# Optimization experiments

Hardware: AMD Instinct MI355X
Metric: run time of the kernel (lower is better)

The kernel has to match this reference:

```python
import jax, jax.numpy as jnp
import numpy as np
from jax import lax

B, S, T = 128, 512, 256


def setup_inputs() -> dict:
    key = jax.random.key(0)
    k1, k2, k3, k4, k5, k6 = jax.random.split(key, 6)
    logits = jax.random.normal(k1, (B, S, T), dtype=jnp.float32)
    lengths = jax.random.randint(k2, (B,), S // 2, S + 1)
    mask = jnp.arange(S)[None, :] < lengths[:, None]  # [B,S] bool, mask[:,0] always True
    labels = jax.random.randint(k3, (B, S), 0, T)
    start_transitions = 0.1 * jax.random.normal(k4, (T,), dtype=jnp.float32)
    end_transitions = 0.1 * jax.random.normal(k5, (T,), dtype=jnp.float32)
    transitions = 0.1 * jax.random.normal(k6, (T, T), dtype=jnp.float32)
    return {"logits": logits, "mask": mask, "labels": labels,
            "start_transitions": start_transitions,
            "end_transitions": end_transitions,
            "transitions": transitions}


def _numerator(logits, tags, mask, start_t, end_t, trans):
    # Score of the gold tag path (torchcrf _compute_score), fully vectorized.
    b = jnp.arange(logits.shape[0])
    maskf = mask.astype(logits.dtype)
    emit = jnp.take_along_axis(logits, tags[..., None], axis=2)[..., 0]  # [B,S]
    score = start_t[tags[:, 0]] + emit[:, 0]
    tr = trans[tags[:, :-1], tags[:, 1:]]  # [B,S-1]
    score = score + jnp.sum((tr + emit[:, 1:]) * maskf[:, 1:], axis=1)
    lengths = mask.sum(axis=1)
    last_tags = tags[b, lengths - 1]
    return score + end_t[last_tags]


def _denominator(logits, mask, start_t, end_t, trans):
    # Forward algorithm (log partition), lax.scan over time.
    score0 = start_t[None, :] + logits[:, 0]  # [B,T]

    def step(score, xs):
        emit, m = xs  # emit [B,T], m [B]
        nxt = jax.nn.logsumexp(score[:, :, None] + trans[None, :, :]
                               + emit[:, None, :], axis=1)  # [B,T]
        return jnp.where(m[:, None], nxt, score), None

    emits = jnp.swapaxes(logits[:, 1:], 0, 1)  # [S-1,B,T]
    masks = mask[:, 1:].T  # [S-1,B]
    score, _ = lax.scan(step, score0, (emits, masks))
    return jax.nn.logsumexp(score + end_t[None, :], axis=1)  # [B]


def _viterbi(logits, mask, start_t, end_t, trans):
    # Viterbi decode with masking; masked steps carry score and use identity
    # backpointers so backtracing passes through padding correctly.
    Bn, Sn, Tn = logits.shape
    score0 = start_t[None, :] + logits[:, 0]  # [B,T]
    ident = jnp.arange(Tn, dtype=jnp.int32)[None, :]

    def step(score, xs):
        emit, m = xs
        cand = score[:, :, None] + trans[None, :, :]  # [B,T_prev,T_next]
        idx = jnp.argmax(cand, axis=1).astype(jnp.int32)  # [B,T]
        nxt = jnp.max(cand, axis=1) + emit
        score = jnp.where(m[:, None], nxt, score)
        hist = jnp.where(m[:, None], idx, ident)
        return score, hist

    emits = jnp.swapaxes(logits[:, 1:], 0, 1)
    masks = mask[:, 1:].T
    score, history = lax.scan(step, score0, (emits, masks))  # history [S-1,B,T]
    last = jnp.argmax(score + end_t[None, :], axis=1).astype(jnp.int32)  # [B]

    def back(tag, h):
        prev = jnp.take_along_axis(h, tag[:, None], axis=1)[:, 0]
        return prev, prev

    _, tags_prefix = lax.scan(back, last, history, reverse=True)  # [S-1,B]
    tags = jnp.concatenate([tags_prefix.T, last[:, None]], axis=1)  # [B,S]
    return jnp.where(mask, tags, 0)


def reference(logits, mask, labels, start_transitions, end_transitions, transitions):
    pred = _viterbi(logits, mask, start_transitions, end_transitions, transitions)
    num = _numerator(logits, labels, mask, start_transitions, end_transitions, transitions)
    den = _denominator(logits, mask, start_transitions, end_transitions, transitions)
    loss = -jnp.mean(num - den)  # torchcrf reduction='mean', negated
    return pred, loss
```

## Files before the change

### kernel.cpp

```cpp
#include <hip/hip_runtime.h>
#include <hip/hip_bf16.h>
#include <math.h>

#define Bn 128
#define Sn 512
#define Tn 256

typedef float vf32t __attribute__((ext_vector_type(32)));
typedef unsigned int vu16t __attribute__((ext_vector_type(16)));
typedef _Float16 half2_t __attribute__((ext_vector_type(2)));

static __device__ inline float dot2h(unsigned int p, unsigned int e, float acc) {
#if __has_builtin(__builtin_amdgcn_fdot2)
    return __builtin_amdgcn_fdot2(__builtin_bit_cast(half2_t, p),
                                  __builtin_bit_cast(half2_t, e), acc, false);
#else
    half2_t ph = __builtin_bit_cast(half2_t, p), eh = __builtin_bit_cast(half2_t, e);
    return acc + (float)ph.x * (float)eh.x + (float)ph.y * (float)eh.y;
#endif
}


__global__ void prep_kernel(const float* __restrict__ trans, float* __restrict__ transT,
                            _Float16* __restrict__ E16) {
    int k = blockIdx.x * blockDim.x + threadIdx.x;
    int i = k >> 8, c = k & 255;
    float v = trans[k];
    transT[c * 256 + i] = v;
    E16[((size_t)(i >> 1) * 512) + c * 2 + (i & 1)] = (_Float16)__expf(v);
}

__launch_bounds__(512, 2)
__global__ void crf_fwd3_kernel(const float* __restrict__ logits,
                                const float* __restrict__ start_t,
                                const float* __restrict__ end_t,
                                const float* __restrict__ trans,
                                const unsigned int* __restrict__ E16w,
                                const void* __restrict__ mask,
                                const int* __restrict__ labels,
                                int* __restrict__ lengths_out,
                                float* __restrict__ hist,
                                float* __restrict__ den_out,
                                int* __restrict__ last_out,
                                float* __restrict__ num_out) {
    const int bid = blockIdx.x;
    const bool is_vit = bid < Bn;
    const int b = is_vit ? bid : bid - Bn;
    const int tid = threadIdx.x;
    const int jp = tid & 63;
    const int q  = tid >> 6;
    const int j0 = jp * 4;
    const int i0 = q * 32;
    const int wv = tid >> 6, lane = tid & 63;

    __shared__ __align__(16) float sbuf[Tn];
    __shared__ __align__(16) _Float16 p16[Tn];
    __shared__ __align__(16) float part[8 * Tn];
    __shared__ float msh[2];
    __shared__ int   lenred[8];
    __shared__ float wredf[8];
    __shared__ int   wredi[8];
    __shared__ float wnum[8];

    int nz;
    {
        const unsigned int* mu = (const unsigned int*)mask;
        unsigned int w0 = mu[0];
        if (w0 == 1u)                nz = (((const int*)mask)[b * Sn + tid] != 0);
        else if (w0 == 0x3F800000u)  nz = (((const float*)mask)[b * Sn + tid] != 0.0f);
        else                         nz = (((const unsigned char*)mask)[b * Sn + tid] != 0);
    }
    unsigned long long bal = __ballot(nz != 0);
    if (lane == 0) lenred[wv] = __popcll(bal);
    __syncthreads();
    int len = 0;
    #pragma unroll
    for (int w = 0; w < 8; ++w) len += lenred[w];
    if (is_vit && tid == 0) lengths_out[b] = len;

    const float* lg = logits + (size_t)b * Sn * Tn + tid;
    const float4* sb4 = (const float4*)sbuf;
    const unsigned int* p16w = (const unsigned int*)p16;

    float cur = 0.0f, emit_cur = 0.0f, emit_next = 0.0f;

    if (is_vit) {
        vf32t tvA, tvB, tvC, tvD;
        #pragma unroll
        for (int r = 0; r < 32; ++r) {
            float4 v = *(const float4*)(trans + (size_t)(i0 + r) * Tn + j0);
            tvA[r] = v.x; tvB[r] = v.y; tvC[r] = v.z; tvD[r] = v.w;
        }

        if (tid < Tn) {
            cur = start_t[tid] + lg[0];
            sbuf[tid] = cur;
            emit_cur = lg[Tn];
        }
        __syncthreads();

        for (int t = 1; t < len; ++t) {
            if (tid < Tn) {
                int tn = (t + 1 < len) ? (t + 1) : (len - 1);
                emit_next = lg[(size_t)tn * Tn];
            }
            float bA = -INFINITY, bB = -INFINITY, bC = -INFINITY, bD = -INFINITY;
            #pragma unroll
            for (int k = 0; k < 8; ++k) {
                float4 s4 = sb4[q * 8 + k];
                int i = 4 * k;
                float cA0 = s4.x + tvA[i],     cA1 = s4.y + tvA[i + 1];
                float cA2 = s4.z + tvA[i + 2], cA3 = s4.w + tvA[i + 3];
                bA = fmaxf(fmaxf(bA, cA0), cA1); bA = fmaxf(fmaxf(bA, cA2), cA3);
                float cB0 = s4.x + tvB[i],     cB1 = s4.y + tvB[i + 1];
                float cB2 = s4.z + tvB[i + 2], cB3 = s4.w + tvB[i + 3];
                bB = fmaxf(fmaxf(bB, cB0), cB1); bB = fmaxf(fmaxf(bB, cB2), cB3);
                float cC0 = s4.x + tvC[i],     cC1 = s4.y + tvC[i + 1];
                float cC2 = s4.z + tvC[i + 2], cC3 = s4.w + tvC[i + 3];
                bC = fmaxf(fmaxf(bC, cC0), cC1); bC = fmaxf(fmaxf(bC, cC2), cC3);
                float cD0 = s4.x + tvD[i],     cD1 = s4.y + tvD[i + 1];
                float cD2 = s4.z + tvD[i + 2], cD3 = s4.w + tvD[i + 3];
                bD = fmaxf(fmaxf(bD, cD0), cD1); bD = fmaxf(fmaxf(bD, cD2), cD3);
            }
            *(float4*)(part + q * Tn + j0) = make_float4(bA, bB, bC, bD);
            __syncthreads();
            if (tid < Tn) {
                float bb = part[tid];
                #pragma unroll
                for (int q2 = 1; q2 < 8; ++q2) bb = fmaxf(bb, part[q2 * Tn + tid]);
                hist[((size_t)t * Bn + b) * Tn + tid] = bb;
                cur = bb + emit_cur;
                emit_cur = emit_next;
                sbuf[tid] = cur;
            }
            __syncthreads();
        }

        float bv = -INFINITY; int bj = 0;
        if (tid < Tn) { bv = cur + end_t[tid]; bj = tid; }
        #pragma unroll
        for (int off = 32; off; off >>= 1) {
            float ov = __shfl_xor(bv, off);
            int   oj = __shfl_xor(bj, off);
            if (ov > bv || (ov == bv && oj < bj)) { bv = ov; bj = oj; }
        }
        if (lane == 0) { wredf[wv] = bv; wredi[wv] = bj; }
        __syncthreads();
        if (tid == 0) {
            float BB = wredf[0]; int AA = wredi[0];
            #pragma unroll
            for (int w = 1; w < 4; ++w)
                if (wredf[w] > BB || (wredf[w] == BB && wredi[w] < AA)) { BB = wredf[w]; AA = wredi[w]; }
            last_out[b] = AA;
        }
    } else {
        vu16t tdA, tdB, tdC, tdD;
        #pragma unroll
        for (int k = 0; k < 16; ++k) {
            uint4 v = *(const uint4*)(E16w + (size_t)(16 * q + k) * Tn + j0);
            tdA[k] = v.x; tdB[k] = v.y; tdC[k] = v.z; tdD[k] = v.w;
        }

        const float SHIFT = 9.0f;
        float pbase = 0.0f;
        if (tid < Tn) {
            cur = start_t[tid] + lg[0];
            if (tid == 0) msh[0] = cur;
            emit_cur = lg[Tn];
        }
        __syncthreads();
        if (tid < Tn) {
            pbase = msh[0] + SHIFT;
            p16[tid] = (_Float16)__expf(cur - pbase);
        }
        __syncthreads();

        for (int t = 1; t < len; ++t) {
            if (tid < Tn) {
                int tn = (t + 1 < len) ? (t + 1) : (len - 1);
                emit_next = lg[(size_t)tn * Tn];
            }
            float sA = 0.f, sB = 0.f, sC = 0.f, sD = 0.f;
            #pragma unroll
            for (int k = 0; k < 8; ++k) {
                uint2 pp = *(const uint2*)(p16w + q * 16 + 2 * k);
                int i = 2 * k;
                sA = dot2h(pp.x, tdA[i], sA); sA = dot2h(pp.y, tdA[i + 1], sA);
                sB = dot2h(pp.x, tdB[i], sB); sB = dot2h(pp.y, tdB[i + 1], sB);
                sC = dot2h(pp.x, tdC[i], sC); sC = dot2h(pp.y, tdC[i + 1], sC);
                sD = dot2h(pp.x, tdD[i], sD); sD = dot2h(pp.y, tdD[i + 1], sD);
            }
            *(float4*)(part + q * Tn + j0) = make_float4(sA, sB, sC, sD);
            __syncthreads();
            if (tid < Tn) {
                float tot = part[tid];
                #pragma unroll
                for (int q2 = 1; q2 < 8; ++q2) tot += part[q2 * Tn + tid];
                float nb = msh[(t - 1) & 1];
                cur = pbase + __logf(tot) + emit_cur;
                emit_cur = emit_next;
                p16[tid] = (_Float16)__expf(cur - nb - SHIFT);
                pbase = nb + SHIFT;
                if (tid == 0) msh[t & 1] = cur;
            }
            __syncthreads();
        }

        float v2 = (tid < Tn) ? (cur + end_t[tid]) : -INFINITY;
        float wm = v2;
        #pragma unroll
        for (int off = 32; off; off >>= 1) wm = fmaxf(wm, __shfl_xor(wm, off));
        if (lane == 0) wredf[wv] = wm;
        __syncthreads();
        float M = fmaxf(fmaxf(wredf[0], wredf[1]), fmaxf(wredf[2], wredf[3]));
        float ex = (tid < Tn) ? __expf(v2 - M) : 0.0f;
        #pragma unroll
        for (int off = 32; off; off >>= 1) ex += __shfl_xor(ex, off);
        if (lane == 0) wnum[wv] = ex;
        __syncthreads();
        if (tid == 0) den_out[b] = M + __logf(wnum[0] + wnum[1] + wnum[2] + wnum[3]);
        __syncthreads();

        float acc = 0.0f;
        if (tid >= 1 && tid < len) {
            int prev = labels[b * Sn + tid - 1], curl = labels[b * Sn + tid];
            acc = trans[prev * Tn + curl] + logits[((size_t)b * Sn + tid) * Tn + curl];
        }
        #pragma unroll
        for (int off = 32; off; off >>= 1) acc += __shfl_xor(acc, off);
        if (lane == 0) wnum[wv] = acc;
        __syncthreads();
        if (tid == 0) {
            float s = 0.0f;
            #pragma unroll
            for (int w = 0; w < 8; ++w) s += wnum[w];
            int l0 = labels[b * Sn];
            int ll = labels[b * Sn + len - 1];
            num_out[b] = start_t[l0] + logits[(size_t)b * Sn * Tn + l0] + s + end_t[ll];
        }
    }
}

__global__ void bt_loss_kernel(const float* __restrict__ hist,
                               const float* __restrict__ logits,
                               const float* __restrict__ start_t,
                               const float* __restrict__ transT,
                               const int* __restrict__ last,
                               const int* __restrict__ lengths,
                               const float* __restrict__ num,
                               const float* __restrict__ den,
                               float* __restrict__ pred,
                               float* __restrict__ out_loss) {
    const int lane = threadIdx.x;
    if (blockIdx.x == Bn) {
        float v = (den[lane] - num[lane]) + (den[lane + 64] - num[lane + 64]);
        #pragma unroll
        for (int off = 32; off; off >>= 1) v += __shfl_xor(v, off);
        if (lane == 0) out_loss[0] = v * (1.0f / 128.0f);
        return;
    }
    const int b = blockIdx.x;
    const int len = lengths[b], len1 = len - 1;
    __shared__ int tg[Sn];
    int tag = last[b];
    if (lane == 0) tg[len1] = tag;
    float target = hist[((size_t)len1 * Bn + b) * Tn + tag];

    const float4* lgrow = (const float4*)(logits + (size_t)b * Sn * Tn) + lane;
    const char* histb = (const char*)(hist + (size_t)b * Tn);
    float4 s4 = *((const float4*)start_t + lane);

    const int PF = 8;
    float4 hbuf[PF], ebuf[PF];
    #pragma unroll
    for (int qq = 0; qq < PF; ++qq) {
        int r = len1 - 1 - qq;
        if (r >= 0) {
            int rh = (r > 1) ? r : 1;
            ebuf[qq] = lgrow[(size_t)r * 64];
            hbuf[qq] = *((const float4*)(histb + (size_t)rh * (Bn * Tn * 4)) + lane);
        }
    }

    for (int k = 0; k < len1; ++k) {
        int r = len1 - 1 - k;
        float4 t4 = *((const float4*)(transT + (size_t)tag * Tn) + lane);
        float4 h4 = hbuf[k & (PF - 1)], e4 = ebuf[k & (PF - 1)];
        int rp = r - PF;
        if (rp >= 0) {
            int rh = (rp > 1) ? rp : 1;
            ebuf[k & (PF - 1)] = lgrow[(size_t)rp * 64];
            hbuf[k & (PF - 1)] = *((const float4*)(histb + (size_t)rh * (Bn * Tn * 4)) + lane);
        }
        float4 sv;
        if (r > 0) {
            sv.x = h4.x + e4.x; sv.y = h4.y + e4.y; sv.z = h4.z + e4.z; sv.w = h4.w + e4.w;
        } else {
            sv.x = s4.x + e4.x; sv.y = s4.y + e4.y; sv.z = s4.z + e4.z; sv.w = s4.w + e4.w;
        }
        int m4 = ((sv.x + t4.x) == target ? 1 : 0)
               | ((sv.y + t4.y) == target ? 2 : 0)
               | ((sv.z + t4.z) == target ? 4 : 0)
               | ((sv.w + t4.w) == target ? 8 : 0);
        unsigned long long bb = __ballot(m4 != 0);
        int L = __ffsll(bb) - 1;
        int mm = __shfl(m4, L);
        int slot = __ffs(mm) - 1;
        tag = L * 4 + slot;
        if (lane == 0) tg[r] = tag;
        float hv = (slot == 0) ? h4.x : (slot == 1) ? h4.y : (slot == 2) ? h4.z : h4.w;
        target = __shfl(hv, L);
    }
    __syncthreads();
    for (int t = lane; t < Sn; t += 64)
        pred[(size_t)b * Sn + t] = (t < len) ? (float)tg[t] : 0.0f;
}


__global__ void compute_E_kernel(const float* __restrict__ trans, __hip_bfloat16* __restrict__ E) {
    int k = blockIdx.x * blockDim.x + threadIdx.x;
    if (k < Tn * Tn) E[k] = __float2bfloat16(__expf(trans[k]));
}

__global__ void lengths_kernel(const void* __restrict__ mask, int* __restrict__ lengths) {
    int b = blockIdx.x, tid = threadIdx.x;
    const unsigned int* mu = (const unsigned int*)mask;
    unsigned int w0 = mu[0];
    int cnt = 0;
    if (w0 == 1u) {
        const int* mi = (const int*)mask;
        for (int t = tid; t < Sn; t += 256) cnt += (mi[b * Sn + t] != 0);
    } else if (w0 == 0x3F800000u) {
        const float* mf = (const float*)mask;
        for (int t = tid; t < Sn; t += 256) cnt += (mf[b * Sn + t] != 0.0f);
    } else {
        const unsigned char* mb = (const unsigned char*)mask;
        for (int t = tid; t < Sn; t += 256) cnt += (mb[b * Sn + t] != 0);
    }
    for (int off = 32; off; off >>= 1) cnt += __shfl_xor(cnt, off);
    __shared__ int red[4];
    if ((tid & 63) == 0) red[tid >> 6] = cnt;
    __syncthreads();
    if (tid == 0) lengths[b] = red[0] + red[1] + red[2] + red[3];
}

__global__ void numerator_kernel(const float* __restrict__ logits, const int* __restrict__ labels,
                                 const float* __restrict__ start_t, const float* __restrict__ end_t,
                                 const float* __restrict__ trans, const int* __restrict__ lengths,
                                 float* __restrict__ num) {
    int b = blockIdx.x, tid = threadIdx.x;
    int len = lengths[b];
    float acc = 0.0f;
    for (int t = tid + 1; t < len; t += 256) {
        int prev = labels[b * Sn + t - 1], cur = labels[b * Sn + t];
        acc += trans[prev * Tn + cur] + logits[((size_t)b * Sn + t) * Tn + cur];
    }
    for (int off = 32; off; off >>= 1) acc += __shfl_xor(acc, off);
    __shared__ float red[4];
    if ((tid & 63) == 0) red[tid >> 6] = acc;
    __syncthreads();
    if (tid == 0) {
        int l0 = labels[b * Sn];
        int ll = labels[b * Sn + len - 1];
        num[b] = start_t[l0] + logits[(size_t)b * Sn * Tn + l0]
               + red[0] + red[1] + red[2] + red[3] + end_t[ll];
    }
}

__launch_bounds__(1024)
__global__ void fused_fwd_kernel(const float* __restrict__ logits,
                                 const float* __restrict__ start_t,
                                 const float* __restrict__ end_t,
                                 const float* __restrict__ trans,
                                 const __hip_bfloat16* __restrict__ E,
                                 const int* __restrict__ lengths,
                                 unsigned char* __restrict__ hist,
                                 float* __restrict__ den_out,
                                 int* __restrict__ last_out) {
    int b = blockIdx.x;
    int tid = threadIdx.x;
    int j = tid & 255;
    int h = tid >> 8;
    int i0 = h * 64;

    __shared__ __align__(16) float sden[Tn];
    __shared__ __align__(16) float svit[Tn];
    __shared__ __align__(16) float p[Tn];
    __shared__ float redf[16];
    __shared__ float reds[16];
    __shared__ float redb[16];
    __shared__ int   redbi[16];
    __shared__ float pd[1024];
    __shared__ float pv[1024];
    __shared__ int   pa[1024];

    int len = lengths[b];
    if (tid < Tn) {
        float v = start_t[j] + logits[(size_t)b * Sn * Tn + j];
        sden[j] = v;
        svit[j] = v;
    }
    __syncthreads();

    for (int t = 1; t < len; ++t) {
        float v = sden[j];
        for (int off = 32; off; off >>= 1) v = fmaxf(v, __shfl_xor(v, off));
        if ((tid & 63) == 0) redf[tid >> 6] = v;
        __syncthreads();
        float m = redf[0];
        #pragma unroll
        for (int w = 1; w < 16; ++w) m = fmaxf(m, redf[w]);
        if (tid < Tn) p[j] = __expf(sden[j] - m);
        __syncthreads();

        float s = 0.0f, best = -INFINITY;
        int arg = 0;
        const float* tr = trans + (size_t)i0 * Tn + j;
        const __hip_bfloat16* er = E + (size_t)i0 * Tn + j;
        #pragma unroll 4
        for (int i = i0; i < i0 + 64; i += 4) {
            float4 p4  = *(const float4*)(p + i);
            float4 sv4 = *(const float4*)(svit + i);
            float tr0 = tr[0 * Tn], tr1 = tr[1 * Tn], tr2 = tr[2 * Tn], tr3 = tr[3 * Tn];
            float e0 = __bfloat162float(er[0 * Tn]);
            float e1 = __bfloat162float(er[1 * Tn]);
            float e2 = __bfloat162float(er[2 * Tn]);
            float e3 = __bfloat162float(er[3 * Tn]);
            tr += 4 * Tn; er += 4 * Tn;
            s = fmaf(p4.x, e0, s); s = fmaf(p4.y, e1, s);
            s = fmaf(p4.z, e2, s); s = fmaf(p4.w, e3, s);
            float c0 = sv4.x + tr0; if (c0 > best) { best = c0; arg = i + 0; }
            float c1 = sv4.y + tr1; if (c1 > best) { best = c1; arg = i + 1; }
            float c2 = sv4.z + tr2; if (c2 > best) { best = c2; arg = i + 2; }
            float c3 = sv4.w + tr3; if (c3 > best) { best = c3; arg = i + 3; }
        }
        pd[tid] = s; pv[tid] = best; pa[tid] = arg;
        __syncthreads();

        if (tid < Tn) {
            float ss = pd[j] + pd[j + 256] + pd[j + 512] + pd[j + 768];
            float bb = pv[j]; int aa = pa[j];
            if (pv[j + 256] > bb) { bb = pv[j + 256]; aa = pa[j + 256]; }
            if (pv[j + 512] > bb) { bb = pv[j + 512]; aa = pa[j + 512]; }
            if (pv[j + 768] > bb) { bb = pv[j + 768]; aa = pa[j + 768]; }
            float emit = logits[((size_t)b * Sn + t) * Tn + j];
            sden[j] = m + __logf(ss) + emit;
            svit[j] = bb + emit;
            hist[((size_t)t * Bn + b) * Tn + j] = (unsigned char)aa;
        }
        __syncthreads();
    }

    float v2d = sden[j] + end_t[j];
    float M = v2d;
    for (int off = 32; off; off >>= 1) M = fmaxf(M, __shfl_xor(M, off));
    if ((tid & 63) == 0) redf[tid >> 6] = M;
    __syncthreads();
    M = redf[0];
    #pragma unroll
    for (int w = 1; w < 16; ++w) M = fmaxf(M, redf[w]);

    float ex = (tid < Tn) ? __expf(v2d - M) : 0.0f;
    for (int off = 32; off; off >>= 1) ex += __shfl_xor(ex, off);

    float v2v = svit[j] + end_t[j];
    float bv = v2v; int bj = j;
    for (int off = 32; off; off >>= 1) {
        float ov = __shfl_xor(bv, off); int oj = __shfl_xor(bj, off);
        if (ov > bv || (ov == bv && oj < bj)) { bv = ov; bj = oj; }
    }
    if ((tid & 63) == 0) { reds[tid >> 6] = ex; redb[tid >> 6] = bv; redbi[tid >> 6] = bj; }
    __syncthreads();
    if (tid == 0) {
        float sum = 0.0f;
        #pragma unroll
        for (int w = 0; w < 16; ++w) sum += reds[w];
        den_out[b] = M + __logf(sum);
        float BB = redb[0]; int AA = redbi[0];
        #pragma unroll
        for (int w = 1; w < 16; ++w)
            if (redb[w] > BB || (redb[w] == BB && redbi[w] < AA)) { BB = redb[w]; AA = redbi[w]; }
        last_out[b] = AA;
    }
}

__global__ void backtrack_kernel(const unsigned char* __restrict__ hist,
                                 const int* __restrict__ last,
                                 const int* __restrict__ lengths,
                                 float* __restrict__ pred) {
    int b = blockIdx.x, lane = threadIdx.x;
    int len = lengths[b];
    int len1 = len - 1;
    __shared__ int tg[Sn];
    int tag = last[b];

    const int P = 16;
    unsigned int buf[P];
    #pragma unroll
    for (int qq = 0; qq < P; ++qq) {
        int r = len1 - qq;
        if (qq < len1)
            buf[qq] = *(const unsigned int*)(hist + ((size_t)r * Bn + b) * Tn + lane * 4);
    }
    if (lane == 0) tg[len1] = tag;
    for (int qq = 0; qq < len1; ++qq) {
        unsigned int w = buf[qq & (P - 1)];
        int sel = __shfl((int)w, tag >> 2, 64);
        tag = (sel >> ((tag & 3) * 8)) & 255;
        int t = len1 - 1 - qq;
        if (lane == 0) tg[t] = tag;
        int rn = len1 - qq - P;
        if (rn >= 1)
            buf[qq & (P - 1)] = *(const unsigned int*)(hist + ((size_t)rn * Bn + b) * Tn + lane * 4);
    }
    __syncthreads();
    for (int t = lane; t < Sn; t += 64)
        pred[(size_t)b * Sn + t] = (t < len) ? (float)tg[t] : 0.0f;
}

__global__ void loss_kernel(const float* __restrict__ num, const float* __restrict__ den,
                            float* __restrict__ out_loss) {
    int tid = threadIdx.x;
    float v = den[tid] - num[tid];
    for (int off = 32; off; off >>= 1) v += __shfl_xor(v, off);
    __shared__ float r2[2];
    if ((tid & 63) == 0) r2[tid >> 6] = v;
    __syncthreads();
    if (tid == 0) out_loss[0] = (r2[0] + r2[1]) * (1.0f / 128.0f);
}


extern "C" void kernel_launch(void* const* d_in, const int* in_sizes, int n_in,
                              void* d_out, int out_size, void* d_ws, size_t ws_size,
                              hipStream_t stream) {
    const float* logits  = (const float*)d_in[0];
    const void*  mask    = d_in[1];
    const int*   labels  = (const int*)d_in[2];
    const float* start_t = (const float*)d_in[3];
    const float* end_t   = (const float*)d_in[4];
    const float* trans   = (const float*)d_in[5];
    float* out = (float*)d_out;

    char* ws = (char*)d_ws;
    const size_t histF = (size_t)Sn * Bn * Tn * 4;
    const size_t tblF  = (size_t)Tn * Tn * 4;
    const size_t e16F  = (size_t)Tn * Tn * 2;
    const size_t needF = histF + tblF + e16F + 8192;

    if (ws_size >= needF) {
        float*        hist    = (float*)ws;
        float*        transT  = (float*)(ws + histF);
        _Float16*     E16     = (_Float16*)(ws + histF + tblF);
        char*         tail    = ws + histF + tblF + e16F;
        int*          lengths = (int*)tail;
        float*        num     = (float*)(tail + 2048);
        float*        den     = (float*)(tail + 4096);
        int*          lastp   = (int*)(tail + 6144);

        prep_kernel<<<Tn * Tn / 256, 256, 0, stream>>>(trans, transT, E16);
        crf_fwd3_kernel<<<2 * Bn, 512, 0, stream>>>(logits, start_t, end_t, trans,
                                                    (const unsigned int*)E16, mask,
                                                    labels, lengths, hist, den, lastp, num);
        bt_loss_kernel<<<Bn + 1, 64, 0, stream>>>(hist, logits, start_t, transT, lastp,
                                                  lengths, num, den, out, out + (size_t)Bn * Sn);
    } else {
        const size_t histSz = (size_t)Sn * Bn * Tn;
        unsigned char*  hist    = (unsigned char*)ws;
        int*            lengths = (int*)(ws + histSz);
        float*          num     = (float*)(ws + histSz + 512);
        float*          den     = (float*)(ws + histSz + 1024);
        int*            lastp   = (int*)(ws + histSz + 1536);
        __hip_bfloat16* E       = (__hip_bfloat16*)(ws + histSz + 2048);

        compute_E_kernel<<<(Tn * Tn) / 256, 256, 0, stream>>>(trans, E);
        lengths_kernel<<<Bn, 256, 0, stream>>>(mask, lengths);
        fused_fwd_kernel<<<Bn, 1024, 0, stream>>>(logits, start_t, end_t, trans, E,
                                                  lengths, hist, den, lastp);
        numerator_kernel<<<Bn, 256, 0, stream>>>(logits, labels, start_t, end_t, trans,
                                                 lengths, num);
        backtrack_kernel<<<Bn, 64, 0, stream>>>(hist, lastp, lengths, out);
        loss_kernel<<<1, 128, 0, stream>>>(num, den, out + (size_t)Bn * Sn);
    }
}
```

Before: 792.7 us.

## Split forward recursions two ways over source tags and restructure backtrace argmax

The Viterbi and forward-algorithm recursions now give each thread one destination tag and half of the source tags (two partitions) instead of four destination tags across eight partitions. This keeps 128 transition values in registers per thread and shrinks the cross-partition reduction through shared memory from eight terms to two. The backtrace in the loss kernel now unrolls its prefetch ring by the prefetch depth and finds the argmax with four ballots instead of a ballot plus shuffle. The uint8 fallback backtrace drops its prefetch buffer. The trade-off is higher register pressure and a longer serial inner loop per thread.

```diff
diff --git a/kernel.cpp b/kernel.cpp
--- a/kernel.cpp
+++ b/kernel.cpp
@@ -6,8 +6,9 @@
 #define Sn 512
 #define Tn 256
 
-typedef float vf32t __attribute__((ext_vector_type(32)));
-typedef unsigned int vu16t __attribute__((ext_vector_type(16)));
+typedef float vf64 __attribute__((ext_vector_type(64)));
+typedef unsigned int vu64t __attribute__((ext_vector_type(64)));
+typedef float f2 __attribute__((ext_vector_type(2)));
 typedef _Float16 half2_t __attribute__((ext_vector_type(2)));
 
 static __device__ inline float dot2h(unsigned int p, unsigned int e, float acc) {
@@ -31,7 +32,7 @@
 }
 
 __launch_bounds__(512, 2)
-__global__ void crf_fwd3_kernel(const float* __restrict__ logits,
+__global__ void crf_fwd4_kernel(const float* __restrict__ logits,
                                 const float* __restrict__ start_t,
                                 const float* __restrict__ end_t,
                                 const float* __restrict__ trans,
@@ -47,15 +48,13 @@
     const bool is_vit = bid < Bn;
     const int b = is_vit ? bid : bid - Bn;
     const int tid = threadIdx.x;
-    const int jp = tid & 63;
-    const int q  = tid >> 6;
-    const int j0 = jp * 4;
-    const int i0 = q * 32;
+    const int jp = tid & 255;
+    const int q  = tid >> 8;
     const int wv = tid >> 6, lane = tid & 63;
 
     __shared__ __align__(16) float sbuf[Tn];
     __shared__ __align__(16) _Float16 p16[Tn];
-    __shared__ __align__(16) float part[8 * Tn];
+    __shared__ __align__(16) float part[2 * Tn];
     __shared__ float msh[2];
     __shared__ int   lenred[8];
     __shared__ float wredf[8];
@@ -81,15 +80,16 @@
     const float* lg = logits + (size_t)b * Sn * Tn + tid;
     const float4* sb4 = (const float4*)sbuf;
     const unsigned int* p16w = (const unsigned int*)p16;
+    const uint4* p16w4 = (const uint4*)p16;
 
     float cur = 0.0f, emit_cur = 0.0f, emit_next = 0.0f;
 
     if (is_vit) {
-        vf32t tvA, tvB, tvC, tvD;
-        #pragma unroll
-        for (int r = 0; r < 32; ++r) {
-            float4 v = *(const float4*)(trans + (size_t)(i0 + r) * Tn + j0);
-            tvA[r] = v.x; tvB[r] = v.y; tvC[r] = v.z; tvD[r] = v.w;
+        vf64 tA, tB;
+        #pragma unroll
+        for (int r = 0; r < 64; ++r) {
+            tA[r] = trans[(size_t)(128 * q + r) * Tn + jp];
+            tB[r] = trans[(size_t)(128 * q + 64 + r) * Tn + jp];
         }
 
         if (tid < Tn) {
@@ -104,30 +104,29 @@
                 int tn = (t + 1 < len) ? (t + 1) : (len - 1);
                 emit_next = lg[(size_t)tn * Tn];
             }
-            float bA = -INFINITY, bB = -INFINITY, bC = -INFINITY, bD = -INFINITY;
+            float b0 = -INFINITY, b1 = -INFINITY;
             #pragma unroll
-            for (int k = 0; k < 8; ++k) {
-                float4 s4 = sb4[q * 8 + k];
+            for (int k = 0; k < 16; ++k) {
+                float4 s4 = sb4[q * 32 + k];
                 int i = 4 * k;
-                float cA0 = s4.x + tvA[i],     cA1 = s4.y + tvA[i + 1];
-                float cA2 = s4.z + tvA[i + 2], cA3 = s4.w + tvA[i + 3];
-                bA = fmaxf(fmaxf(bA, cA0), cA1); bA = fmaxf(fmaxf(bA, cA2), cA3);
-                float cB0 = s4.x + tvB[i],     cB1 = s4.y + tvB[i + 1];
-                float cB2 = s4.z + tvB[i + 2], cB3 = s4.w + tvB[i + 3];
-                bB = fmaxf(fmaxf(bB, cB0), cB1); bB = fmaxf(fmaxf(bB, cB2), cB3);
-                float cC0 = s4.x + tvC[i],     cC1 = s4.y + tvC[i + 1];
-                float cC2 = s4.z + tvC[i + 2], cC3 = s4.w + tvC[i + 3];
-                bC = fmaxf(fmaxf(bC, cC0), cC1); bC = fmaxf(fmaxf(bC, cC2), cC3);
-                float cD0 = s4.x + tvD[i],     cD1 = s4.y + tvD[i + 1];
-                float cD2 = s4.z + tvD[i + 2], cD3 = s4.w + tvD[i + 3];
-                bD = fmaxf(fmaxf(bD, cD0), cD1); bD = fmaxf(fmaxf(bD, cD2), cD3);
-            }
-            *(float4*)(part + q * Tn + j0) = make_float4(bA, bB, bC, bD);
+                f2 ca = (f2){s4.x, s4.y} + (f2){tA[i], tA[i + 1]};
+                f2 cb = (f2){s4.z, s4.w} + (f2){tA[i + 2], tA[i + 3]};
+                b0 = fmaxf(fmaxf(b0, ca.x), ca.y);
+                b1 = fmaxf(fmaxf(b1, cb.x), cb.y);
+            }
+            #pragma unroll
+            for (int k = 0; k < 16; ++k) {
+                float4 s4 = sb4[q * 32 + 16 + k];
+                int i = 4 * k;
+                f2 ca = (f2){s4.x, s4.y} + (f2){tB[i], tB[i + 1]};
+                f2 cb = (f2){s4.z, s4.w} + (f2){tB[i + 2], tB[i + 3]};
+                b0 = fmaxf(fmaxf(b0, ca.x), ca.y);
+                b1 = fmaxf(fmaxf(b1, cb.x), cb.y);
+            }
+            part[q * Tn + jp] = fmaxf(b0, b1);
             __syncthreads();
             if (tid < Tn) {
-                float bb = part[tid];
-                #pragma unroll
-                for (int q2 = 1; q2 < 8; ++q2) bb = fmaxf(bb, part[q2 * Tn + tid]);
+                float bb = fmaxf(part[tid], part[Tn + tid]);
                 hist[((size_t)t * Bn + b) * Tn + tid] = bb;
                 cur = bb + emit_cur;
                 emit_cur = emit_next;
@@ -154,12 +153,10 @@
             last_out[b] = AA;
         }
     } else {
-        vu16t tdA, tdB, tdC, tdD;
-        #pragma unroll
-        for (int k = 0; k < 16; ++k) {
-            uint4 v = *(const uint4*)(E16w + (size_t)(16 * q + k) * Tn + j0);
-            tdA[k] = v.x; tdB[k] = v.y; tdC[k] = v.z; tdD[k] = v.w;
-        }
+        vu64t td;
+        #pragma unroll
+        for (int k = 0; k < 64; ++k)
+            td[k] = E16w[(size_t)(64 * q + k) * Tn + jp];
 
         const float SHIFT = 9.0f;
         float pbase = 0.0f;
@@ -180,22 +177,18 @@
                 int tn = (t + 1 < len) ? (t + 1) : (len - 1);
                 emit_next = lg[(size_t)tn * Tn];
             }
-            float sA = 0.f, sB = 0.f, sC = 0.f, sD = 0.f;
+            float sA = 0.f, sB = 0.f;
             #pragma unroll
-            for (int k = 0; k < 8; ++k) {
-                uint2 pp = *(const uint2*)(p16w + q * 16 + 2 * k);
-                int i = 2 * k;
-                sA = dot2h(pp.x, tdA[i], sA); sA = dot2h(pp.y, tdA[i + 1], sA);
-                sB = dot2h(pp.x, tdB[i], sB); sB = dot2h(pp.y, tdB[i + 1], sB);
-                sC = dot2h(pp.x, tdC[i], sC); sC = dot2h(pp.y, tdC[i + 1], sC);
-                sD = dot2h(pp.x, tdD[i], sD); sD = dot2h(pp.y, tdD[i + 1], sD);
-            }
-            *(float4*)(part + q * Tn + j0) = make_float4(sA, sB, sC, sD);
+            for (int k = 0; k < 16; ++k) {
+                uint4 pp = p16w4[q * 16 + k];
+                int i = 4 * k;
+                sA = dot2h(pp.x, td[i],     sA); sB = dot2h(pp.y, td[i + 1], sB);
+                sA = dot2h(pp.z, td[i + 2], sA); sB = dot2h(pp.w, td[i + 3], sB);
+            }
+            part[q * Tn + jp] = sA + sB;
             __syncthreads();
             if (tid < Tn) {
-                float tot = part[tid];
-                #pragma unroll
-                for (int q2 = 1; q2 < 8; ++q2) tot += part[q2 * Tn + tid];
+                float tot = part[tid] + part[Tn + tid];
                 float nb = msh[(t - 1) & 1];
                 cur = pbase + __logf(tot) + emit_cur;
                 emit_cur = emit_next;
@@ -273,43 +266,50 @@
     const int PF = 8;
     float4 hbuf[PF], ebuf[PF];
     #pragma unroll
-    for (int qq = 0; qq < PF; ++qq) {
-        int r = len1 - 1 - qq;
+    for (int u = 0; u < PF; ++u) {
+        int r = len1 - 1 - u;
         if (r >= 0) {
             int rh = (r > 1) ? r : 1;
-            ebuf[qq] = lgrow[(size_t)r * 64];
-            hbuf[qq] = *((const float4*)(histb + (size_t)rh * (Bn * Tn * 4)) + lane);
-        }
-    }
-
-    for (int k = 0; k < len1; ++k) {
-        int r = len1 - 1 - k;
-        float4 t4 = *((const float4*)(transT + (size_t)tag * Tn) + lane);
-        float4 h4 = hbuf[k & (PF - 1)], e4 = ebuf[k & (PF - 1)];
-        int rp = r - PF;
-        if (rp >= 0) {
-            int rh = (rp > 1) ? rp : 1;
-            ebuf[k & (PF - 1)] = lgrow[(size_t)rp * 64];
-            hbuf[k & (PF - 1)] = *((const float4*)(histb + (size_t)rh * (Bn * Tn * 4)) + lane);
-        }
-        float4 sv;
-        if (r > 0) {
-            sv.x = h4.x + e4.x; sv.y = h4.y + e4.y; sv.z = h4.z + e4.z; sv.w = h4.w + e4.w;
-        } else {
-            sv.x = s4.x + e4.x; sv.y = s4.y + e4.y; sv.z = s4.z + e4.z; sv.w = s4.w + e4.w;
-        }
-        int m4 = ((sv.x + t4.x) == target ? 1 : 0)
-               | ((sv.y + t4.y) == target ? 2 : 0)
-               | ((sv.z + t4.z) == target ? 4 : 0)
-               | ((sv.w + t4.w) == target ? 8 : 0);
-        unsigned long long bb = __ballot(m4 != 0);
-        int L = __ffsll(bb) - 1;
-        int mm = __shfl(m4, L);
-        int slot = __ffs(mm) - 1;
-        tag = L * 4 + slot;
-        if (lane == 0) tg[r] = tag;
-        float hv = (slot == 0) ? h4.x : (slot == 1) ? h4.y : (slot == 2) ? h4.z : h4.w;
-        target = __shfl(hv, L);
+            ebuf[u] = lgrow[(size_t)r * 64];
+            hbuf[u] = *((const float4*)(histb + (size_t)rh * (Bn * Tn * 4)) + lane);
+        }
+    }
+
+    for (int k0 = 0; k0 < len1; k0 += PF) {
+        #pragma unroll
+        for (int u = 0; u < PF; ++u) {
+            int k = k0 + u;
+            if (k < len1) {
+                int r = len1 - 1 - k;
+                float4 t4 = *((const float4*)(transT + (size_t)tag * Tn) + lane);
+                float4 h4 = hbuf[u], e4 = ebuf[u];
+                int rp = r - PF;
+                if (rp >= 0) {
+                    int rh = (rp > 1) ? rp : 1;
+                    ebuf[u] = lgrow[(size_t)rp * 64];
+                    hbuf[u] = *((const float4*)(histb + (size_t)rh * (Bn * Tn * 4)) + lane);
+                }
+                float4 sv;
+                if (r > 0) {
+                    sv.x = h4.x + e4.x; sv.y = h4.y + e4.y; sv.z = h4.z + e4.z; sv.w = h4.w + e4.w;
+                } else {
+                    sv.x = s4.x + e4.x; sv.y = s4.y + e4.y; sv.z = s4.z + e4.z; sv.w = s4.w + e4.w;
+                }
+                unsigned long long B0 = __ballot((sv.x + t4.x) == target);
+                unsigned long long B1 = __ballot((sv.y + t4.y) == target);
+                unsigned long long B2 = __ballot((sv.z + t4.z) == target);
+                unsigned long long B3 = __ballot((sv.w + t4.w) == target);
+                int c0 = B0 ? ((__ffsll(B0) - 1) * 4 + 0) : 1024;
+                int c1 = B1 ? ((__ffsll(B1) - 1) * 4 + 1) : 1024;
+                int c2 = B2 ? ((__ffsll(B2) - 1) * 4 + 2) : 1024;
+                int c3 = B3 ? ((__ffsll(B3) - 1) * 4 + 3) : 1024;
+                tag = min(min(c0, c1), min(c2, c3));
+                if (lane == 0) tg[r] = tag;
+                int L = tag >> 2, slot = tag & 3;
+                float hv = (slot == 0) ? h4.x : (slot == 1) ? h4.y : (slot == 2) ? h4.z : h4.w;
+                target = __shfl(hv, L);
+            }
+        }
     }
     __syncthreads();
     for (int t = lane; t < Sn; t += 64)
@@ -494,24 +494,13 @@
     __shared__ int tg[Sn];
     int tag = last[b];
 
-    const int P = 16;
-    unsigned int buf[P];
-    #pragma unroll
-    for (int qq = 0; qq < P; ++qq) {
-        int r = len1 - qq;
-        if (qq < len1)
-            buf[qq] = *(const unsigned int*)(hist + ((size_t)r * Bn + b) * Tn + lane * 4);
-    }
     if (lane == 0) tg[len1] = tag;
     for (int qq = 0; qq < len1; ++qq) {
-        unsigned int w = buf[qq & (P - 1)];
+        int r = len1 - qq;
+        unsigned int w = *(const unsigned int*)(hist + ((size_t)r * Bn + b) * Tn + lane * 4);
         int sel = __shfl((int)w, tag >> 2, 64);
         tag = (sel >> ((tag & 3) * 8)) & 255;
-        int t = len1 - 1 - qq;
-        if (lane == 0) tg[t] = tag;
-        int rn = len1 - qq - P;
-        if (rn >= 1)
-            buf[qq & (P - 1)] = *(const unsigned int*)(hist + ((size_t)rn * Bn + b) * Tn + lane * 4);
+        if (lane == 0) tg[r - 1] = tag;
     }
     __syncthreads();
     for (int t = lane; t < Sn; t += 64)
@@ -558,7 +547,7 @@
         int*          lastp   = (int*)(tail + 6144);
 
         prep_kernel<<<Tn * Tn / 256, 256, 0, stream>>>(trans, transT, E16);
-        crf_fwd3_kernel<<<2 * Bn, 512, 0, stream>>>(logits, start_t, end_t, trans,
+        crf_fwd4_kernel<<<2 * Bn, 512, 0, stream>>>(logits, start_t, end_t, trans,
                                                     (const unsigned int*)E16, mask,
                                                     labels, lengths, hist, den, lastp, num);
         bt_loss_kernel<<<Bn + 1, 64, 0, stream>>>(hist, logits, start_t, transT, lastp,
```

After: 814.3 us. 1.03x slower.

## Prune Viterbi max with transition-range candidate filtering and fuse backtrace

Applied to the files above, without the earlier changes.

Computes the global range of the transition matrix, then at each Viterbi step considers only previous states whose score lies within that range of the maximum. Whenever at most 64 states qualify, each output tag scans only those candidates rather than all 256. Backpointers are stored as 8-bit indices and the backtrace runs inside the forward kernel, which removes the float history buffer and the separate backtrack kernel. This adds a range-reduction kernel and extra barriers and ballots every step, and on steps with many candidates it falls back to a full scan that reads trans from global memory instead of registers.

```diff
diff --git a/kernel.cpp b/kernel.cpp
--- a/kernel.cpp
+++ b/kernel.cpp
@@ -6,7 +6,6 @@
 #define Sn 512
 #define Tn 256
 
-typedef float vf32t __attribute__((ext_vector_type(32)));
 typedef unsigned int vu16t __attribute__((ext_vector_type(16)));
 typedef _Float16 half2_t __attribute__((ext_vector_type(2)));
 
@@ -21,46 +20,79 @@
 }
 
 
-__global__ void prep_kernel(const float* __restrict__ trans, float* __restrict__ transT,
-                            _Float16* __restrict__ E16) {
-    int k = blockIdx.x * blockDim.x + threadIdx.x;
+__global__ void prep_kernel(const float* __restrict__ trans, _Float16* __restrict__ E16,
+                            float* __restrict__ rngmin, float* __restrict__ rngmax) {
+    int blk = blockIdx.x, tid = threadIdx.x;
+    int k = blk * 256 + tid;
     int i = k >> 8, c = k & 255;
     float v = trans[k];
-    transT[c * 256 + i] = v;
-    E16[((size_t)(i >> 1) * 512) + c * 2 + (i & 1)] = (_Float16)__expf(v);
+    E16[(size_t)(i >> 1) * 512 + c * 2 + (i & 1)] = (_Float16)__expf(v);
+    float mn = v, mx = v;
+    #pragma unroll
+    for (int off = 32; off; off >>= 1) {
+        mn = fminf(mn, __shfl_xor(mn, off));
+        mx = fmaxf(mx, __shfl_xor(mx, off));
+    }
+    __shared__ float smn[4], smx[4];
+    if ((tid & 63) == 0) { smn[tid >> 6] = mn; smx[tid >> 6] = mx; }
+    __syncthreads();
+    if (tid == 0) {
+        rngmin[blk] = fminf(fminf(smn[0], smn[1]), fminf(smn[2], smn[3]));
+        rngmax[blk] = fmaxf(fmaxf(smx[0], smx[1]), fmaxf(smx[2], smx[3]));
+    }
+}
+
+__global__ void range_kernel(const float* __restrict__ rngmin, const float* __restrict__ rngmax,
+                             float* __restrict__ Rout) {
+    int tid = threadIdx.x;
+    float mn = rngmin[tid], mx = rngmax[tid];
+    #pragma unroll
+    for (int off = 32; off; off >>= 1) {
+        mn = fminf(mn, __shfl_xor(mn, off));
+        mx = fmaxf(mx, __shfl_xor(mx, off));
+    }
+    __shared__ float smn[4], smx[4];
+    if ((tid & 63) == 0) { smn[tid >> 6] = mn; smx[tid >> 6] = mx; }
+    __syncthreads();
+    if (tid == 0) {
+        float MN = fminf(fminf(smn[0], smn[1]), fminf(smn[2], smn[3]));
+        float MX = fmaxf(fmaxf(smx[0], smx[1]), fmaxf(smx[2], smx[3]));
+        Rout[0] = (MX - MN) * 1.000001f + 1e-6f;
+    }
 }
 
 __launch_bounds__(512, 2)
-__global__ void crf_fwd3_kernel(const float* __restrict__ logits,
+__global__ void crf_fwd5_kernel(const float* __restrict__ logits,
                                 const float* __restrict__ start_t,
                                 const float* __restrict__ end_t,
                                 const float* __restrict__ trans,
                                 const unsigned int* __restrict__ E16w,
                                 const void* __restrict__ mask,
                                 const int* __restrict__ labels,
-                                int* __restrict__ lengths_out,
-                                float* __restrict__ hist,
+                                const float* __restrict__ Rptr,
+                                unsigned char* __restrict__ hist8,
                                 float* __restrict__ den_out,
-                                int* __restrict__ last_out,
-                                float* __restrict__ num_out) {
+                                float* __restrict__ num_out,
+                                float* __restrict__ pred) {
     const int bid = blockIdx.x;
     const bool is_vit = bid < Bn;
     const int b = is_vit ? bid : bid - Bn;
     const int tid = threadIdx.x;
-    const int jp = tid & 63;
-    const int q  = tid >> 6;
-    const int j0 = jp * 4;
-    const int i0 = q * 32;
     const int wv = tid >> 6, lane = tid & 63;
 
     __shared__ __align__(16) float sbuf[Tn];
     __shared__ __align__(16) _Float16 p16[Tn];
     __shared__ __align__(16) float part[8 * Tn];
+    __shared__ float candv[64];
+    __shared__ int   cand[64];
+    __shared__ int   ccnt[8];
     __shared__ float msh[2];
-    __shared__ int   lenred[8];
     __shared__ float wredf[8];
     __shared__ int   wredi[8];
     __shared__ float wnum[8];
+    __shared__ int   lenred[8];
+    __shared__ int   tg[Sn];
+    __shared__ int   lastSh;
 
     int nz;
     {
@@ -70,74 +102,83 @@
         else if (w0 == 0x3F800000u)  nz = (((const float*)mask)[b * Sn + tid] != 0.0f);
         else                         nz = (((const unsigned char*)mask)[b * Sn + tid] != 0);
     }
-    unsigned long long bal = __ballot(nz != 0);
-    if (lane == 0) lenred[wv] = __popcll(bal);
+    unsigned long long bal0 = __ballot(nz != 0);
+    if (lane == 0) lenred[wv] = __popcll(bal0);
     __syncthreads();
     int len = 0;
     #pragma unroll
     for (int w = 0; w < 8; ++w) len += lenred[w];
-    if (is_vit && tid == 0) lengths_out[b] = len;
-
-    const float* lg = logits + (size_t)b * Sn * Tn + tid;
-    const float4* sb4 = (const float4*)sbuf;
-    const unsigned int* p16w = (const unsigned int*)p16;
-
-    float cur = 0.0f, emit_cur = 0.0f, emit_next = 0.0f;
 
     if (is_vit) {
-        vf32t tvA, tvB, tvC, tvD;
-        #pragma unroll
-        for (int r = 0; r < 32; ++r) {
-            float4 v = *(const float4*)(trans + (size_t)(i0 + r) * Tn + j0);
-            tvA[r] = v.x; tvB[r] = v.y; tvC[r] = v.z; tvD[r] = v.w;
-        }
-
-        if (tid < Tn) {
-            cur = start_t[tid] + lg[0];
-            sbuf[tid] = cur;
-            emit_cur = lg[Tn];
-        }
-        __syncthreads();
+        const int j = tid & 255;
+        const float R = Rptr[0];
+        const float* lg = logits + (size_t)b * Sn * Tn + j;
+
+        float cur = start_t[j] + lg[0];
+        float emit_cur = lg[Tn];
+        float emit_next = 0.0f;
+        if (tid < Tn) sbuf[j] = cur;
 
         for (int t = 1; t < len; ++t) {
-            if (tid < Tn) {
+            {
                 int tn = (t + 1 < len) ? (t + 1) : (len - 1);
                 emit_next = lg[(size_t)tn * Tn];
             }
-            float bA = -INFINITY, bB = -INFINITY, bC = -INFINITY, bD = -INFINITY;
+            float wm = cur;
             #pragma unroll
-            for (int k = 0; k < 8; ++k) {
-                float4 s4 = sb4[q * 8 + k];
-                int i = 4 * k;
-                float cA0 = s4.x + tvA[i],     cA1 = s4.y + tvA[i + 1];
-                float cA2 = s4.z + tvA[i + 2], cA3 = s4.w + tvA[i + 3];
-                bA = fmaxf(fmaxf(bA, cA0), cA1); bA = fmaxf(fmaxf(bA, cA2), cA3);
-                float cB0 = s4.x + tvB[i],     cB1 = s4.y + tvB[i + 1];
-                float cB2 = s4.z + tvB[i + 2], cB3 = s4.w + tvB[i + 3];
-                bB = fmaxf(fmaxf(bB, cB0), cB1); bB = fmaxf(fmaxf(bB, cB2), cB3);
-                float cC0 = s4.x + tvC[i],     cC1 = s4.y + tvC[i + 1];
-                float cC2 = s4.z + tvC[i + 2], cC3 = s4.w + tvC[i + 3];
-                bC = fmaxf(fmaxf(bC, cC0), cC1); bC = fmaxf(fmaxf(bC, cC2), cC3);
-                float cD0 = s4.x + tvD[i],     cD1 = s4.y + tvD[i + 1];
-                float cD2 = s4.z + tvD[i + 2], cD3 = s4.w + tvD[i + 3];
-                bD = fmaxf(fmaxf(bD, cD0), cD1); bD = fmaxf(fmaxf(bD, cD2), cD3);
-            }
-            *(float4*)(part + q * Tn + j0) = make_float4(bA, bB, bC, bD);
+            for (int off = 32; off; off >>= 1) wm = fmaxf(wm, __shfl_xor(wm, off));
+            int flag = (cur >= wm - R) ? 1 : 0;
+            unsigned long long bal = __ballot(flag);
+            if (lane == 0) ccnt[wv] = __popcll(bal);
             __syncthreads();
-            if (tid < Tn) {
-                float bb = part[tid];
+            int K = ccnt[0] + ccnt[1] + ccnt[2] + ccnt[3];
+            if (tid < Tn && flag && K <= 64) {
+                int base = 0;
                 #pragma unroll
-                for (int q2 = 1; q2 < 8; ++q2) bb = fmaxf(bb, part[q2 * Tn + tid]);
-                hist[((size_t)t * Bn + b) * Tn + tid] = bb;
-                cur = bb + emit_cur;
-                emit_cur = emit_next;
-                sbuf[tid] = cur;
+                for (int w = 0; w < 4; ++w) if (w < wv) base += ccnt[w];
+                int rank = base + __popcll(bal & (((unsigned long long)1 << lane) - 1));
+                cand[rank] = j;
+                candv[rank] = cur;
             }
             __syncthreads();
-        }
-
-        float bv = -INFINITY; int bj = 0;
-        if (tid < Tn) { bv = cur + end_t[tid]; bj = tid; }
+
+            float best = -INFINITY; int arg = 0;
+            if (K <= 64) {
+                for (int k0 = 0; k0 < K; k0 += 16) {
+                    float tv[16];
+                    #pragma unroll
+                    for (int u = 0; u < 16; ++u)
+                        if (k0 + u < K) tv[u] = trans[(size_t)cand[k0 + u] * Tn + j];
+                    #pragma unroll
+                    for (int u = 0; u < 16; ++u)
+                        if (k0 + u < K) {
+                            float c = candv[k0 + u] + tv[u];
+                            if (c > best) { best = c; arg = cand[k0 + u]; }
+                        }
+                }
+            } else {
+                for (int k0 = 0; k0 < Tn; k0 += 16) {
+                    float tv[16], cv[16];
+                    #pragma unroll
+                    for (int u = 0; u < 16; ++u) {
+                        tv[u] = trans[(size_t)(k0 + u) * Tn + j];
+                        cv[u] = sbuf[k0 + u];
+                    }
+                    #pragma unroll
+                    for (int u = 0; u < 16; ++u) {
+                        float c = cv[u] + tv[u];
+                        if (c > best) { best = c; arg = k0 + u; }
+                    }
+                }
+            }
+            if (tid < Tn) hist8[((size_t)t * Bn + b) * Tn + j] = (unsigned char)arg;
+            cur = best + emit_cur;
+            emit_cur = emit_next;
+            if (tid < Tn) sbuf[j] = cur;
+        }
+
+        float bv = (tid < Tn) ? (cur + end_t[j]) : -INFINITY;
+        int bj = (tid < Tn) ? j : 0;
         #pragma unroll
         for (int off = 32; off; off >>= 1) {
             float ov = __shfl_xor(bv, off);
@@ -151,9 +192,42 @@
             #pragma unroll
             for (int w = 1; w < 4; ++w)
                 if (wredf[w] > BB || (wredf[w] == BB && wredi[w] < AA)) { BB = wredf[w]; AA = wredi[w]; }
-            last_out[b] = AA;
-        }
+            lastSh = AA;
+        }
+        __syncthreads();
+        __threadfence();
+
+        if (wv == 0) {
+            int len1 = len - 1;
+            int tag = lastSh;
+            const int P = 16;
+            unsigned int buf[P];
+            #pragma unroll
+            for (int q = 0; q < P; ++q) {
+                int r = len1 - q;
+                if (q < len1)
+                    buf[q] = *(const unsigned int*)(hist8 + ((size_t)r * Bn + b) * Tn + lane * 4);
+            }
+            if (lane == 0) tg[len1] = tag;
+            for (int q = 0; q < len1; ++q) {
+                unsigned int w = buf[q & (P - 1)];
+                int sel = __shfl((int)w, tag >> 2, 64);
+                tag = (sel >> ((tag & 3) * 8)) & 255;
+                if (lane == 0) tg[len1 - 1 - q] = tag;
+                int rn = len1 - q - P;
+                if (rn >= 1)
+                    buf[q & (P - 1)] = *(const unsigned int*)(hist8 + ((size_t)rn * Bn + b) * Tn + lane * 4);
+            }
+        }
+        __syncthreads();
+        pred[(size_t)b * Sn + tid] = (tid < len) ? (float)tg[tid] : 0.0f;
     } else {
+        const int jp = tid & 63;
+        const int q  = tid >> 6;
+        const int j0 = jp * 4;
+        const float* lg = logits + (size_t)b * Sn * Tn + tid;
+        const unsigned int* p16w = (const unsigned int*)p16;
+
         vu16t tdA, tdB, tdC, tdD;
         #pragma unroll
         for (int k = 0; k < 16; ++k) {
@@ -162,7 +236,7 @@
         }
 
         const float SHIFT = 9.0f;
-        float pbase = 0.0f;
+        float cur = 0.0f, emit_cur = 0.0f, emit_next = 0.0f, pbase = 0.0f;
         if (tid < Tn) {
             cur = start_t[tid] + lg[0];
             if (tid == 0) msh[0] = cur;
@@ -241,79 +315,15 @@
     }
 }
 
-__global__ void bt_loss_kernel(const float* __restrict__ hist,
-                               const float* __restrict__ logits,
-                               const float* __restrict__ start_t,
-                               const float* __restrict__ transT,
-                               const int* __restrict__ last,
-                               const int* __restrict__ lengths,
-                               const float* __restrict__ num,
-                               const float* __restrict__ den,
-                               float* __restrict__ pred,
-                               float* __restrict__ out_loss) {
-    const int lane = threadIdx.x;
-    if (blockIdx.x == Bn) {
-        float v = (den[lane] - num[lane]) + (den[lane + 64] - num[lane + 64]);
-        #pragma unroll
-        for (int off = 32; off; off >>= 1) v += __shfl_xor(v, off);
-        if (lane == 0) out_loss[0] = v * (1.0f / 128.0f);
-        return;
-    }
-    const int b = blockIdx.x;
-    const int len = lengths[b], len1 = len - 1;
-    __shared__ int tg[Sn];
-    int tag = last[b];
-    if (lane == 0) tg[len1] = tag;
-    float target = hist[((size_t)len1 * Bn + b) * Tn + tag];
-
-    const float4* lgrow = (const float4*)(logits + (size_t)b * Sn * Tn) + lane;
-    const char* histb = (const char*)(hist + (size_t)b * Tn);
-    float4 s4 = *((const float4*)start_t + lane);
-
-    const int PF = 8;
-    float4 hbuf[PF], ebuf[PF];
-    #pragma unroll
-    for (int qq = 0; qq < PF; ++qq) {
-        int r = len1 - 1 - qq;
-        if (r >= 0) {
-            int rh = (r > 1) ? r : 1;
-            ebuf[qq] = lgrow[(size_t)r * 64];
-            hbuf[qq] = *((const float4*)(histb + (size_t)rh * (Bn * Tn * 4)) + lane);
-        }
-    }
-
-    for (int k = 0; k < len1; ++k) {
-        int r = len1 - 1 - k;
-        float4 t4 = *((const float4*)(transT + (size_t)tag * Tn) + lane);
-        float4 h4 = hbuf[k & (PF - 1)], e4 = ebuf[k & (PF - 1)];
-        int rp = r - PF;
-        if (rp >= 0) {
-            int rh = (rp > 1) ? rp : 1;
-            ebuf[k & (PF - 1)] = lgrow[(size_t)rp * 64];
-            hbuf[k & (PF - 1)] = *((const float4*)(histb + (size_t)rh * (Bn * Tn * 4)) + lane);
-        }
-        float4 sv;
-        if (r > 0) {
-            sv.x = h4.x + e4.x; sv.y = h4.y + e4.y; sv.z = h4.z + e4.z; sv.w = h4.w + e4.w;
-        } else {
-            sv.x = s4.x + e4.x; sv.y = s4.y + e4.y; sv.z = s4.z + e4.z; sv.w = s4.w + e4.w;
-        }
-        int m4 = ((sv.x + t4.x) == target ? 1 : 0)
-               | ((sv.y + t4.y) == target ? 2 : 0)
-               | ((sv.z + t4.z) == target ? 4 : 0)
-               | ((sv.w + t4.w) == target ? 8 : 0);
-        unsigned long long bb = __ballot(m4 != 0);
-        int L = __ffsll(bb) - 1;
-        int mm = __shfl(m4, L);
-        int slot = __ffs(mm) - 1;
-        tag = L * 4 + slot;
-        if (lane == 0) tg[r] = tag;
-        float hv = (slot == 0) ? h4.x : (slot == 1) ? h4.y : (slot == 2) ? h4.z : h4.w;
-        target = __shfl(hv, L);
-    }
-    __syncthreads();
-    for (int t = lane; t < Sn; t += 64)
-        pred[(size_t)b * Sn + t] = (t < len) ? (float)tg[t] : 0.0f;
+__global__ void loss_kernel(const float* __restrict__ num, const float* __restrict__ den,
+                            float* __restrict__ out_loss) {
+    int tid = threadIdx.x;
+    float v = den[tid] - num[tid];
+    for (int off = 32; off; off >>= 1) v += __shfl_xor(v, off);
+    __shared__ float r2[2];
+    if ((tid & 63) == 0) r2[tid >> 6] = v;
+    __syncthreads();
+    if (tid == 0) out_loss[0] = (r2[0] + r2[1]) * (1.0f / 128.0f);
 }
 
 
@@ -518,17 +528,6 @@
         pred[(size_t)b * Sn + t] = (t < len) ? (float)tg[t] : 0.0f;
 }
 
-__global__ void loss_kernel(const float* __restrict__ num, const float* __restrict__ den,
-                            float* __restrict__ out_loss) {
-    int tid = threadIdx.x;
-    float v = den[tid] - num[tid];
-    for (int off = 32; off; off >>= 1) v += __shfl_xor(v, off);
-    __shared__ float r2[2];
-    if ((tid & 63) == 0) r2[tid >> 6] = v;
-    __syncthreads();
-    if (tid == 0) out_loss[0] = (r2[0] + r2[1]) * (1.0f / 128.0f);
-}
-
 
 extern "C" void kernel_launch(void* const* d_in, const int* in_sizes, int n_in,
                               void* d_out, int out_size, void* d_ws, size_t ws_size,
@@ -542,27 +541,26 @@
     float* out = (float*)d_out;
 
     char* ws = (char*)d_ws;
-    const size_t histF = (size_t)Sn * Bn * Tn * 4;
-    const size_t tblF  = (size_t)Tn * Tn * 4;
-    const size_t e16F  = (size_t)Tn * Tn * 2;
-    const size_t needF = histF + tblF + e16F + 8192;
+    const size_t hist8Sz = (size_t)Sn * Bn * Tn;
+    const size_t e16F    = (size_t)Tn * Tn * 2;
+    const size_t needF   = hist8Sz + e16F + 16384;
 
     if (ws_size >= needF) {
-        float*        hist    = (float*)ws;
-        float*        transT  = (float*)(ws + histF);
-        _Float16*     E16     = (_Float16*)(ws + histF + tblF);
-        char*         tail    = ws + histF + tblF + e16F;
-        int*          lengths = (int*)tail;
-        float*        num     = (float*)(tail + 2048);
-        float*        den     = (float*)(tail + 4096);
-        int*          lastp   = (int*)(tail + 6144);
-
-        prep_kernel<<<Tn * Tn / 256, 256, 0, stream>>>(trans, transT, E16);
-        crf_fwd3_kernel<<<2 * Bn, 512, 0, stream>>>(logits, start_t, end_t, trans,
-                                                    (const unsigned int*)E16, mask,
-                                                    labels, lengths, hist, den, lastp, num);
-        bt_loss_kernel<<<Bn + 1, 64, 0, stream>>>(hist, logits, start_t, transT, lastp,
-                                                  lengths, num, den, out, out + (size_t)Bn * Sn);
+        unsigned char* hist8  = (unsigned char*)ws;
+        _Float16*      E16    = (_Float16*)(ws + hist8Sz);
+        char*          tail   = ws + hist8Sz + e16F;
+        float*         rngmin = (float*)tail;
+        float*         rngmax = (float*)(tail + 1024);
+        float*         Rout   = (float*)(tail + 2048);
+        float*         num    = (float*)(tail + 4096);
+        float*         den    = (float*)(tail + 6144);
+
+        prep_kernel<<<256, 256, 0, stream>>>(trans, E16, rngmin, rngmax);
+        range_kernel<<<1, 256, 0, stream>>>(rngmin, rngmax, Rout);
+        crf_fwd5_kernel<<<2 * Bn, 512, 0, stream>>>(logits, start_t, end_t, trans,
+                                                    (const unsigned int*)E16, mask, labels,
+                                                    Rout, hist8, den, num, out);
+        loss_kernel<<<1, 128, 0, stream>>>(num, den, out + (size_t)Bn * Sn);
     } else {
         const size_t histSz = (size_t)Sn * Bn * Tn;
         unsigned char*  hist    = (unsigned char*)ws;
```

Measured after the change: 1.826 ms. 130% more time.
